# Kernel optimization log

Hardware: AMD Instinct MI355X
Metric: run time of the kernel (lower is better)

## Reference

```python
import jax, jax.numpy as jnp
import numpy as np

B = 8192          # batch (tokens)
D_LAT = 1024      # latent_dim
D_EMB = 1024      # embed_dim
D = D_LAT + D_EMB # input_dim = 2048
E = 8             # num_experts
K = 2             # top-k


def setup_inputs() -> dict:
    key = jax.random.key(0)
    ks = jax.random.split(key, 6)
    s = 1.0 / np.sqrt(D)  # PyTorch nn.Linear init bound
    return {
        "x": jax.random.normal(ks[0], (B, D_LAT), dtype=jnp.float32),
        "y": jax.random.normal(ks[1], (B, D_EMB), dtype=jnp.float32),
        # expert Linear weights [E, out=D, in=D] and biases [E, D]
        "W_experts": jax.random.uniform(ks[2], (E, D, D), jnp.float32, -s, s),
        "b_experts": jax.random.uniform(ks[3], (E, D), jnp.float32, -s, s),
        # gate Linear weight [E, D] and bias [E]
        "W_gate": jax.random.uniform(ks[4], (E, D), jnp.float32, -s, s),
        "b_gate": jax.random.uniform(ks[5], (E,), jnp.float32, -s, s),
    }


def reference(x, y, W_experts, b_experts, W_gate, b_gate):
    # inp: [B, D]
    inp = jnp.concatenate([x, y], axis=1)
    # gating (eval mode: no noise): [B, E]
    gate_logits = inp @ W_gate.T + b_gate
    # top-k values/indices (sorted descending, matching torch.topk): [B, K]
    topk_val, topk_idx = jax.lax.top_k(gate_logits, K)
    topk_gates = jax.nn.softmax(topk_val, axis=1)  # [B, K]
    # dense all-expert outputs, matching original per-expert loop: [B, E, D]
    all_out = jnp.einsum('bd,eod->beo', inp, W_experts) + b_experts[None, :, :]
    # gather top-k expert outputs: [B, K, D]
    topk_out = jnp.take_along_axis(all_out, topk_idx[:, :, None], axis=1)
    # gate-weighted combine: [B, D]
    fused = jnp.sum(topk_out * topk_gates[:, :, None], axis=1)
    return fused
```

## Files before the change

kernel.cpp:

```cpp
#include <hip/hip_runtime.h>
#include <stdint.h>

typedef __attribute__((ext_vector_type(4))) float f32x4;
typedef __attribute__((ext_vector_type(8))) short short8v;
typedef __attribute__((ext_vector_type(8))) unsigned short ushort8v;
typedef __attribute__((ext_vector_type(4))) unsigned short ushort4v;

#define NB 8192
#define ND 2048
#define NE 8
#define NT 32

__device__ __forceinline__ unsigned short f2bf(float f) {
    union { float f; uint32_t u; } c; c.f = f;
    uint32_t u = c.u;
    u = u + 0x7FFFu + ((u >> 16) & 1u);
    return (unsigned short)(u >> 16);
}

__global__ __launch_bounds__(256) void cvt_w_kernel(const float* __restrict__ W,
                                                    unsigned short* __restrict__ Wb) {
    size_t i = ((size_t)blockIdx.x * 256 + threadIdx.x) * 8;
    float4 a = *(const float4*)(W + i);
    float4 b = *(const float4*)(W + i + 4);
    ushort8v o;
    o[0] = f2bf(a.x); o[1] = f2bf(a.y); o[2] = f2bf(a.z); o[3] = f2bf(a.w);
    o[4] = f2bf(b.x); o[5] = f2bf(b.y); o[6] = f2bf(b.z); o[7] = f2bf(b.w);
    *(ushort8v*)(Wb + i) = o;
}

__global__ __launch_bounds__(256) void gatecvt_kernel(const float* __restrict__ x,
                                                      const float* __restrict__ y,
                                                      const float* __restrict__ Wg,
                                                      const float* __restrict__ bg,
                                                      unsigned short* __restrict__ inpb,
                                                      int* __restrict__ tkidx,
                                                      float* __restrict__ tkg) {
    const int wave = threadIdx.x >> 6, lane = threadIdx.x & 63;
    const int b = blockIdx.x * 4 + wave;
    const float* xb = x + (size_t)b * 1024;
    const float* yb = y + (size_t)b * 1024;
    unsigned short* ob = inpb + (size_t)b * ND;
    double acc[NE] = {0, 0, 0, 0, 0, 0, 0, 0};
#pragma unroll
    for (int it = 0; it < 8; it++) {
        const int d = it * 256 + lane * 4;
        float4 v = (it < 4) ? *(const float4*)(xb + d) : *(const float4*)(yb + (d - 1024));
        ushort4v o;
        o[0] = f2bf(v.x); o[1] = f2bf(v.y); o[2] = f2bf(v.z); o[3] = f2bf(v.w);
        *(ushort4v*)(ob + d) = o;
#pragma unroll
        for (int e = 0; e < NE; e++) {
            float4 w = *(const float4*)(Wg + e * ND + d);
            acc[e] += (double)v.x * (double)w.x + (double)v.y * (double)w.y
                    + (double)v.z * (double)w.z + (double)v.w * (double)w.w;
        }
    }
#pragma unroll
    for (int e = 0; e < NE; e++) {
        double s = acc[e];
#pragma unroll
        for (int o = 32; o >= 1; o >>= 1) s += __shfl_xor(s, o, 64);
        acc[e] = s;
    }
    if (lane == 0) {
        double v0 = -1e300, v1 = -1e300; int i0 = 0, i1 = 1;
#pragma unroll
        for (int e = 0; e < NE; e++) {
            double val = acc[e] + (double)bg[e];
            if (val > v0)      { v1 = v0; i1 = i0; v0 = val; i0 = e; }
            else if (val > v1) { v1 = val; i1 = e; }
        }
        double e1 = exp(v1 - v0);
        double inv = 1.0 / (1.0 + e1);
        tkidx[b * 2]     = i0;
        tkidx[b * 2 + 1] = i1;
        tkg[b * 2]       = (float)inv;
        tkg[b * 2 + 1]   = (float)(e1 * inv);
    }
}

__global__ __launch_bounds__(256) void hist_kernel(const int* __restrict__ tkidx,
                                                   int* __restrict__ hist) {
    const int p = blockIdx.x * 256 + threadIdx.x;
    const int wave = threadIdx.x >> 6, lane = threadIdx.x & 63;
    const int e = tkidx[p];
    __shared__ int cnt[4][8];
#pragma unroll
    for (int e2 = 0; e2 < 8; e2++) {
        unsigned long long m = __ballot(e == e2);
        if (lane == e2) cnt[wave][e2] = __popcll(m);
    }
    __syncthreads();
    if (threadIdx.x < 8)
        hist[blockIdx.x * 8 + threadIdx.x] =
            cnt[0][threadIdx.x] + cnt[1][threadIdx.x] + cnt[2][threadIdx.x] + cnt[3][threadIdx.x];
}

__global__ void scan_kernel(const int* __restrict__ hist, int* __restrict__ chunkbase,
                            int* __restrict__ meta) {
    __shared__ int total[8], off[8];
    const int t = threadIdx.x;
    if (t < 8) {
        int run = 0;
        for (int c = 0; c < 64; c++) { chunkbase[c * 8 + t] = run; run += hist[c * 8 + t]; }
        total[t] = run; meta[t] = run;
    }
    __syncthreads();
    if (t == 0) { int o = 0; for (int e = 0; e < 8; e++) { off[e] = o; meta[8 + e] = o; o += total[e]; } }
    __syncthreads();
    for (int i = t; i < 512; i += 64) chunkbase[i] += off[i & 7];
}

__global__ __launch_bounds__(256) void fill_kernel(const int* __restrict__ tkidx,
                                                   const float* __restrict__ tkg,
                                                   const int* __restrict__ chunkbase,
                                                   int* __restrict__ tok,
                                                   float* __restrict__ gat) {
    const int p = blockIdx.x * 256 + threadIdx.x;
    const int wave = threadIdx.x >> 6, lane = threadIdx.x & 63;
    const int e = tkidx[p];
    const float g = tkg[p];
    __shared__ int cnt[4][8];
    unsigned long long mym = 0;
#pragma unroll
    for (int e2 = 0; e2 < 8; e2++) {
        unsigned long long m = __ballot(e == e2);
        if (e == e2) mym = m;
        if (lane == e2) cnt[wave][e2] = __popcll(m);
    }
    __syncthreads();
    int basep = chunkbase[blockIdx.x * 8 + e];
    for (int w = 0; w < wave; w++) basep += cnt[w][e];
    const int rank = __popcll(mym & ((1ull << lane) - 1ull));
    tok[basep + rank] = p >> 1;
    gat[basep + rank] = g;
}

#define GLD16(gp, lp) __builtin_amdgcn_global_load_lds( \
    (const __attribute__((address_space(1))) uint32_t*)(gp), \
    (__attribute__((address_space(3))) uint32_t*)(lp), 16, 0, 0)

__global__ __launch_bounds__(512, 2) void moe_gemm_kernel(
    const unsigned short* __restrict__ Ab,
    const unsigned short* __restrict__ Wb,
    const float* __restrict__ bias,
    const int* __restrict__ tok,
    const float* __restrict__ gat,
    const int* __restrict__ meta,
    float* __restrict__ out)
{
    const int e = blockIdx.z;
    const int cnt = meta[e];
    const int row0 = blockIdx.y * 256;
    if (row0 >= cnt) return;
    const int col0 = blockIdx.x * 256;
    const int base = meta[8 + e];

    __shared__ __align__(16) unsigned short S[2][4][128][64];

    const int tid  = threadIdx.x;
    const int wv   = tid >> 6;
    const int lane = tid & 63;
    const int wr = wv >> 2, wcn = wv & 3;
    const int fr = lane & 15, kh = lane >> 4;

    const int srow = tid >> 3;
    const int cg8  = ((tid & 7) ^ (srow & 7)) * 8;
    const unsigned short* wbase = Wb + (size_t)e * ND * ND;
    const unsigned short* aptr[2][2];
    const unsigned short* bptr[2][2];
#pragma unroll
    for (int h = 0; h < 2; h++)
#pragma unroll
        for (int i = 0; i < 2; i++) {
            int rt = h * 128 + i * 64 + srow;
            int gr = row0 + rt; if (gr > cnt - 1) gr = cnt - 1;
            aptr[h][i] = Ab + (size_t)tok[base + gr] * ND + cg8;
            bptr[h][i] = wbase + (size_t)(col0 + rt) * ND + cg8;
        }

#define STAGE_A(SB, SM, SK) do { \
    GLD16(aptr[SM][0] + (SK), (char*)&S[SB][SM][0][0] + tid * 16); \
    GLD16(aptr[SM][1] + (SK), (char*)&S[SB][SM][0][0] + tid * 16 + 8192); } while (0)
#define STAGE_B(SB, SN, SK) do { \
    GLD16(bptr[SN][0] + (SK), (char*)&S[SB][2 + SN][0][0] + tid * 16); \
    GLD16(bptr[SN][1] + (SK), (char*)&S[SB][2 + SN][0][0] + tid * 16 + 8192); } while (0)

    f32x4 acc[8][4];
#pragma unroll
    for (int m = 0; m < 8; m++)
#pragma unroll
        for (int n = 0; n < 4; n++) acc[m][n] = f32x4{0.f, 0.f, 0.f, 0.f};

    const int arow = wr * 64 + fr;
    int ca[2];
#pragma unroll
    for (int ks = 0; ks < 2; ks++) ca[ks] = ((ks * 4 + kh) ^ (fr & 7)) * 8;

    short8v br[4];

#define PH_FULL(PB, PM, KS, ...) do { \
    short8v ar[4]; \
    _Pragma("unroll") \
    for (int ml = 0; ml < 4; ml++) \
        ar[ml] = *(const short8v*)&S[PB][PM][arow + ml * 16][ca[KS]]; \
    _Pragma("unroll") \
    for (int n = 0; n < 4; n++) \
        br[n] = *(const short8v*)&S[PB][2 + (n >> 1)][wcn * 32 + (n & 1) * 16 + fr][ca[KS]]; \
    __VA_ARGS__; \
    __builtin_amdgcn_sched_barrier(0); \
    __builtin_amdgcn_s_barrier(); \
    asm volatile("s_waitcnt lgkmcnt(0)" ::: "memory"); \
    __builtin_amdgcn_sched_barrier(0); \
    __builtin_amdgcn_s_setprio(1); \
    _Pragma("unroll") \
    for (int ml = 0; ml < 4; ml++) \
        _Pragma("unroll") \
        for (int n = 0; n < 4; n++) \
            acc[PM * 4 + ml][n] = __builtin_amdgcn_mfma_f32_16x16x32_bf16( \
                ar[ml], br[n], acc[PM * 4 + ml][n], 0, 0, 0); \
    __builtin_amdgcn_s_setprio(0); \
    __builtin_amdgcn_sched_barrier(0); \
    __builtin_amdgcn_s_barrier(); \
} while (0)

#define PH_REUSE(PB, PM, KS, ...) do { \
    short8v ar[4]; \
    _Pragma("unroll") \
    for (int ml = 0; ml < 4; ml++) \
        ar[ml] = *(const short8v*)&S[PB][PM][arow + ml * 16][ca[KS]]; \
    __VA_ARGS__; \
    __builtin_amdgcn_sched_barrier(0); \
    __builtin_amdgcn_s_barrier(); \
    asm volatile("s_waitcnt lgkmcnt(0)" ::: "memory"); \
    __builtin_amdgcn_sched_barrier(0); \
    __builtin_amdgcn_s_setprio(1); \
    _Pragma("unroll") \
    for (int ml = 0; ml < 4; ml++) \
        _Pragma("unroll") \
        for (int n = 0; n < 4; n++) \
            acc[PM * 4 + ml][n] = __builtin_amdgcn_mfma_f32_16x16x32_bf16( \
                ar[ml], br[n], acc[PM * 4 + ml][n], 0, 0, 0); \
    __builtin_amdgcn_s_setprio(0); \
    __builtin_amdgcn_sched_barrier(0); \
    __builtin_amdgcn_s_barrier(); \
} while (0)

    STAGE_A(0, 0, 0);
    STAGE_B(0, 0, 0);
    STAGE_B(0, 1, 0);
    STAGE_A(0, 1, 0);
    STAGE_A(1, 0, 64);
    asm volatile("s_waitcnt vmcnt(2)" ::: "memory");
    __builtin_amdgcn_sched_barrier(0);
    __builtin_amdgcn_s_barrier();

    int buf = 0;
    for (int t = 0; t < NT; t++) {
        const int nb = buf ^ 1;
        const int kt1 = (t + 1) * 64;
        const int kt2 = (t + 2) * 64;
        PH_FULL (buf, 0, 0, { if (t + 1 < NT) STAGE_A(nb, 1, kt1); });
        PH_REUSE(buf, 1, 0, { if (t + 1 < NT) STAGE_B(nb, 0, kt1); });
        PH_FULL (buf, 0, 1, { if (t + 1 < NT) STAGE_B(nb, 1, kt1); });
        PH_REUSE(buf, 1, 1, { if (t + 2 < NT) STAGE_A(buf, 0, kt2); });
        if (t + 1 < NT) {
            if (t == NT - 2) asm volatile("s_waitcnt vmcnt(0)" ::: "memory");
            else             asm volatile("s_waitcnt vmcnt(2)" ::: "memory");
            __builtin_amdgcn_sched_barrier(0);
            __builtin_amdgcn_s_barrier();
        }
        buf = nb;
    }

    int   coln[4];
    float bv[4];
#pragma unroll
    for (int n = 0; n < 4; n++) {
        coln[n] = col0 + (n >> 1) * 128 + wcn * 32 + (n & 1) * 16 + fr;
        bv[n] = bias[e * ND + coln[n]];
    }
#pragma unroll
    for (int m = 0; m < 8; m++) {
        const int rbase = row0 + (m >> 2) * 128 + wr * 64 + (m & 3) * 16 + kh * 4;
#pragma unroll
        for (int j = 0; j < 4; j++) {
            const int R = rbase + j;
            if (R < cnt) {
                const int tkn = tok[base + R];
                const float g = gat[base + R];
                float* orow = out + (size_t)tkn * ND;
#pragma unroll
                for (int n = 0; n < 4; n++)
                    atomicAdd(orow + coln[n], g * (acc[m][n][j] + bv[n]));
            }
        }
    }
#undef PH_FULL
#undef PH_REUSE
#undef STAGE_A
#undef STAGE_B
}

extern "C" void kernel_launch(void* const* d_in, const int* in_sizes, int n_in,
                              void* d_out, int out_size, void* d_ws, size_t ws_size,
                              hipStream_t stream) {
    const float* x  = (const float*)d_in[0];
    const float* y  = (const float*)d_in[1];
    const float* We = (const float*)d_in[2];
    const float* be = (const float*)d_in[3];
    const float* Wg = (const float*)d_in[4];
    const float* bg = (const float*)d_in[5];
    float* out = (float*)d_out;

    char* ws = (char*)d_ws;
    int*   meta  = (int*)ws;
    int*   hist  = (int*)(ws + 256);
    int*   cbase = (int*)(ws + 256 + 2048);
    int*   tkidx = (int*)(ws + 8192);
    float* tkg   = (float*)(ws + 8192 + 65536);
    int*   tok   = (int*)(ws + 8192 + 2 * 65536);
    float* gat   = (float*)(ws + 8192 + 3 * 65536);
    unsigned short* inpb = (unsigned short*)(ws + 8192 + 4 * 65536);
    unsigned short* wb   = (unsigned short*)(ws + 8192 + 4 * 65536 + (size_t)NB * ND * 2);

    (void)hipMemsetAsync(d_out, 0, (size_t)NB * ND * sizeof(float), stream);
    cvt_w_kernel<<<16384, 256, 0, stream>>>(We, wb);
    gatecvt_kernel<<<2048, 256, 0, stream>>>(x, y, Wg, bg, inpb, tkidx, tkg);
    hist_kernel<<<64, 256, 0, stream>>>(tkidx, hist);
    scan_kernel<<<1, 64, 0, stream>>>(hist, cbase, meta);
    fill_kernel<<<64, 256, 0, stream>>>(tkidx, tkg, cbase, tok, gat);
    moe_gemm_kernel<<<dim3(8, 32, 8), 512, 0, stream>>>(inpb, wb, be, tok, gat, meta, out);
}
```

Measured before the change: 334.0 us.

## Replace atomic scatter with plain stores into two partial buffers plus combine

Each (token, k) pair now writes its gated expert output with plain stores, into out for k=0 and into a separate workspace buffer for k=1. A combine kernel then adds the two buffers, replacing the output memset and the float atomicAdds. The tok array now holds the pair index, so the slot can be recovered from its low bit. Global-to-LDS staging for the next tile is also moved into the first phase instead of being spread across three. This costs an extra 64MB buffer plus a read-modify-write pass over the output, and falls back to the atomic path if the workspace is too small.

```diff
diff --git a/kernel.cpp b/kernel.cpp
--- a/kernel.cpp
+++ b/kernel.cpp
@@ -133,14 +133,27 @@
     int basep = chunkbase[blockIdx.x * 8 + e];
     for (int w = 0; w < wave; w++) basep += cnt[w][e];
     const int rank = __popcll(mym & ((1ull << lane) - 1ull));
-    tok[basep + rank] = p >> 1;
+    tok[basep + rank] = p;
     gat[basep + rank] = g;
+}
+
+__global__ __launch_bounds__(256) void combine_kernel(float* __restrict__ out,
+                                                      const float* __restrict__ part1) {
+    const size_t stride = (size_t)gridDim.x * 256 * 4;
+    for (size_t i = ((size_t)blockIdx.x * 256 + threadIdx.x) * 4;
+         i < (size_t)NB * ND; i += stride) {
+        f32x4 a = *(const f32x4*)(out + i);
+        f32x4 b = *(const f32x4*)(part1 + i);
+        a = a + b;
+        *(f32x4*)(out + i) = a;
+    }
 }
 
 #define GLD16(gp, lp) __builtin_amdgcn_global_load_lds( \
     (const __attribute__((address_space(1))) uint32_t*)(gp), \
     (__attribute__((address_space(3))) uint32_t*)(lp), 16, 0, 0)
 
+template <bool STORE>
 __global__ __launch_bounds__(512, 2) void moe_gemm_kernel(
     const unsigned short* __restrict__ Ab,
     const unsigned short* __restrict__ Wb,
@@ -148,7 +161,8 @@
     const int* __restrict__ tok,
     const float* __restrict__ gat,
     const int* __restrict__ meta,
-    float* __restrict__ out)
+    float* __restrict__ out0,
+    float* __restrict__ out1)
 {
     const int e = blockIdx.z;
     const int cnt = meta[e];
@@ -176,7 +190,7 @@
         for (int i = 0; i < 2; i++) {
             int rt = h * 128 + i * 64 + srow;
             int gr = row0 + rt; if (gr > cnt - 1) gr = cnt - 1;
-            aptr[h][i] = Ab + (size_t)tok[base + gr] * ND + cg8;
+            aptr[h][i] = Ab + (size_t)(tok[base + gr] >> 1) * ND + cg8;
             bptr[h][i] = wbase + (size_t)(col0 + rt) * ND + cg8;
         }
 
@@ -261,9 +275,9 @@
         const int nb = buf ^ 1;
         const int kt1 = (t + 1) * 64;
         const int kt2 = (t + 2) * 64;
-        PH_FULL (buf, 0, 0, { if (t + 1 < NT) STAGE_A(nb, 1, kt1); });
-        PH_REUSE(buf, 1, 0, { if (t + 1 < NT) STAGE_B(nb, 0, kt1); });
-        PH_FULL (buf, 0, 1, { if (t + 1 < NT) STAGE_B(nb, 1, kt1); });
+        PH_FULL (buf, 0, 0, { if (t + 1 < NT) { STAGE_A(nb, 1, kt1); STAGE_B(nb, 0, kt1); STAGE_B(nb, 1, kt1); } });
+        PH_REUSE(buf, 1, 0, {});
+        PH_FULL (buf, 0, 1, {});
         PH_REUSE(buf, 1, 1, { if (t + 2 < NT) STAGE_A(buf, 0, kt2); });
         if (t + 1 < NT) {
             if (t == NT - 2) asm volatile("s_waitcnt vmcnt(0)" ::: "memory");
@@ -288,12 +302,15 @@
         for (int j = 0; j < 4; j++) {
             const int R = rbase + j;
             if (R < cnt) {
-                const int tkn = tok[base + R];
+                const int pr = tok[base + R];
                 const float g = gat[base + R];
-                float* orow = out + (size_t)tkn * ND;
-#pragma unroll
-                for (int n = 0; n < 4; n++)
-                    atomicAdd(orow + coln[n], g * (acc[m][n][j] + bv[n]));
+                float* orow = ((STORE && (pr & 1)) ? out1 : out0) + (size_t)(pr >> 1) * ND;
+#pragma unroll
+                for (int n = 0; n < 4; n++) {
+                    const float v = g * (acc[m][n][j] + bv[n]);
+                    if (STORE) orow[coln[n]] = v;
+                    else       atomicAdd(&orow[coln[n]], v);
+                }
             }
         }
     }
@@ -322,14 +339,25 @@
     float* tkg   = (float*)(ws + 8192 + 65536);
     int*   tok   = (int*)(ws + 8192 + 2 * 65536);
     float* gat   = (float*)(ws + 8192 + 3 * 65536);
-    unsigned short* inpb = (unsigned short*)(ws + 8192 + 4 * 65536);
-    unsigned short* wb   = (unsigned short*)(ws + 8192 + 4 * 65536 + (size_t)NB * ND * 2);
-
-    (void)hipMemsetAsync(d_out, 0, (size_t)NB * ND * sizeof(float), stream);
+    const size_t off_inpb = 8192 + 4 * 65536;
+    const size_t off_wb   = off_inpb + (size_t)NB * ND * 2;
+    const size_t off_p1   = off_wb + (size_t)NE * ND * ND * 2;
+    const size_t needed   = off_p1 + (size_t)NB * ND * 4;
+    unsigned short* inpb = (unsigned short*)(ws + off_inpb);
+    unsigned short* wb   = (unsigned short*)(ws + off_wb);
+    float*          part1 = (float*)(ws + off_p1);
+    const bool store_mode = (ws_size >= needed);
+
     cvt_w_kernel<<<16384, 256, 0, stream>>>(We, wb);
     gatecvt_kernel<<<2048, 256, 0, stream>>>(x, y, Wg, bg, inpb, tkidx, tkg);
     hist_kernel<<<64, 256, 0, stream>>>(tkidx, hist);
     scan_kernel<<<1, 64, 0, stream>>>(hist, cbase, meta);
     fill_kernel<<<64, 256, 0, stream>>>(tkidx, tkg, cbase, tok, gat);
-    moe_gemm_kernel<<<dim3(8, 32, 8), 512, 0, stream>>>(inpb, wb, be, tok, gat, meta, out);
-}
+    if (store_mode) {
+        moe_gemm_kernel<true><<<dim3(8, 32, 8), 512, 0, stream>>>(inpb, wb, be, tok, gat, meta, out, part1);
+        combine_kernel<<<2048, 256, 0, stream>>>(out, part1);
+    } else {
+        (void)hipMemsetAsync(d_out, 0, (size_t)NB * ND * sizeof(float), stream);
+        moe_gemm_kernel<false><<<dim3(8, 32, 8), 512, 0, stream>>>(inpb, wb, be, tok, gat, meta, out, out);
+    }
+}
```

After: 305.2 us. 1.09x faster.
